# Optimization experiments

Hardware: AMD Instinct MI355X
Metric: run time of the kernel (lower is better)

The kernel has to match this reference:

```python
import jax, jax.numpy as jnp
import numpy as np

BIT = 8          # mantissa bits (incl. sign) for both weights and activations
BLK = 32         # block size along channel dim
QMAX = 2.0 ** (BIT - 1) - 1  # 127
EPS_BN = 1e-5


def bfp_quant(x, bit=BIT, blk=BLK):
    """BFPActivation: block-floating-point quantization of activations.
    Channels are grouped in blocks of `blk`; each block shares the exponent of
    its max-magnitude element, mantissas are rounded to `bit` bits (STE)."""
    N, C, H, W = x.shape
    xb = x.reshape(N, C // blk, blk, H, W)
    max_abs = jnp.max(jnp.abs(xb), axis=2, keepdims=True)
    e = jnp.floor(jnp.log2(jnp.maximum(max_abs, 1e-24)))  # shared exponent
    delta = jnp.exp2(e - (bit - 2))                        # quantization step
    q = jnp.clip(jnp.round(xb / delta), -(2.0 ** (bit - 1)), 2.0 ** (bit - 1) - 1) * delta
    q = q.reshape(N, C, H, W)
    return x + jax.lax.stop_gradient(q - x)  # straight-through


def w_quant(w, bit=BIT, blk=BLK):
    """DSConv2d weight quantization: per (out-channel, in-channel-block, kh, kw)
    float scale (KDS) with `bit`-bit integer mantissa (VQK)."""
    O, I, kh, kw = w.shape
    wb = w.reshape(O, I // blk, blk, kh, kw)
    alpha = jnp.maximum(jnp.max(jnp.abs(wb), axis=2, keepdims=True) / QMAX, 1e-24)
    q = (jnp.round(wb / alpha) * alpha).reshape(O, I, kh, kw)
    return w + jax.lax.stop_gradient(q - w)


def conv(x, w, stride=1, padding=0):
    return jax.lax.conv_general_dilated(
        x, w, (stride, stride), [(padding, padding)] * 2,
        dimension_numbers=("NCHW", "OIHW", "NCHW"))


def bn(x, g, b, m, v):
    # inference-mode BatchNorm2d with running stats
    inv = g / jnp.sqrt(v + EPS_BN)
    return x * inv[None, :, None, None] + (b - m * inv)[None, :, None, None]


def setup_inputs() -> dict:
    key = jax.random.key(0)
    ks = jax.random.split(key, 8)
    N, Cin, H, W_ = 64, 512, 28, 28
    width, Cout = 128, 512
    d = {}
    d["x"] = jax.random.normal(ks[0], (N, Cin, H, W_), jnp.float32)
    d["w1"] = jax.random.normal(ks[1], (width, Cin, 1, 1), jnp.float32) / np.sqrt(Cin)
    d["w2"] = jax.random.normal(ks[2], (width, width, 3, 3), jnp.float32) / np.sqrt(width * 9)
    d["w3"] = jax.random.normal(ks[3], (Cout, width, 1, 1), jnp.float32) / np.sqrt(width)
    for i, c in ((1, width), (2, width), (3, Cout)):
        kk = jax.random.split(jax.random.fold_in(key, i), 4)
        d[f"bn{i}_g"] = 1.0 + 0.1 * jax.random.normal(kk[0], (c,), jnp.float32)
        d[f"bn{i}_b"] = 0.1 * jax.random.normal(kk[1], (c,), jnp.float32)
        d[f"bn{i}_m"] = 0.1 * jax.random.normal(kk[2], (c,), jnp.float32)
        d[f"bn{i}_v"] = 0.5 + jax.random.uniform(kk[3], (c,), jnp.float32)
    return d


def reference(x, w1, w2, w3,
              bn1_g, bn1_b, bn1_m, bn1_v,
              bn2_g, bn2_b, bn2_m, bn2_v,
              bn3_g, bn3_b, bn3_m, bn3_v):
    identity = x
    out = conv(x, w_quant(w1))                       # 1x1, C 512->128
    out = bfp_quant(jax.nn.relu(bn(out, bn1_g, bn1_b, bn1_m, bn1_v)))
    out = conv(out, w_quant(w2), stride=1, padding=1)  # 3x3, C 128->128
    out = bfp_quant(jax.nn.relu(bn(out, bn2_g, bn2_b, bn2_m, bn2_v)))
    out = conv(out, w_quant(w3))                     # 1x1, C 128->512
    out = bn(out, bn3_g, bn3_b, bn3_m, bn3_v)
    out = out + identity
    # seq = Sequential(relu, activation2) in the source (final=False)
    out = bfp_quant(jax.nn.relu(out))
    return out
```

## Files before the change

### kernel.cpp

```cpp
#include <hip/hip_runtime.h>
#include <math.h>


#define HW 784
#define WW 28
#define PTOT 50176

typedef short s8v __attribute__((ext_vector_type(8)));
typedef float f4v __attribute__((ext_vector_type(4)));

__device__ __forceinline__ f4v mfma16(s8v a, s8v b, f4v c) {
  return __builtin_amdgcn_mfma_f32_16x16x32_bf16(a, b, c, 0, 0, 0);
}

__device__ __forceinline__ unsigned short f2bf(float f) {
  unsigned u = __float_as_uint(f);
  u += 0x7fffu + ((u >> 16) & 1u);
  return (unsigned short)(u >> 16);
}
__device__ __forceinline__ float bf2f(unsigned short h) {
  return __uint_as_float(((unsigned)h) << 16);
}

__global__ void wq1_kernel(const float* __restrict__ w, unsigned short* __restrict__ wd) {
  int task = blockIdx.x * blockDim.x + threadIdx.x;
  if (task >= 128 * 16) return;
  int cb = task & 15, o = task >> 4;
  const float* src = w + o * 512 + cb * 32;
  float vals[32], mx = 0.f;
#pragma unroll
  for (int j = 0; j < 32; ++j) { vals[j] = src[j]; mx = fmaxf(mx, fabsf(vals[j])); }
  float alpha = fmaxf(__fdiv_rn(mx, 127.0f), 1e-24f);
#pragma unroll
  for (int j = 0; j < 32; ++j) {
    unsigned short q = f2bf(__fmul_rn(rintf(__fdiv_rn(vals[j], alpha)), alpha));
    wd[o * 1024 + (cb * 32 + j) * 2] = q;
    wd[o * 1024 + (cb * 32 + j) * 2 + 1] = q;
  }
}

__global__ void wq2_kernel(const float* __restrict__ w, unsigned short* __restrict__ wd) {
  int task = blockIdx.x * blockDim.x + threadIdx.x;
  if (task >= 128 * 36) return;
  int o = task / 36, rem = task % 36;
  int khw = rem % 9, cb = rem / 9;
  float vals[32], mx = 0.f;
#pragma unroll
  for (int j = 0; j < 32; ++j) {
    vals[j] = w[(o * 128 + cb * 32 + j) * 9 + khw];
    mx = fmaxf(mx, fabsf(vals[j]));
  }
  float alpha = fmaxf(__fdiv_rn(mx, 127.0f), 1e-24f);
#pragma unroll
  for (int j = 0; j < 32; ++j)
    wd[o * 1152 + khw * 128 + cb * 32 + j] =
        f2bf(__fmul_rn(rintf(__fdiv_rn(vals[j], alpha)), alpha));
}

__global__ void wq3_kernel(const float* __restrict__ w, unsigned short* __restrict__ wd) {
  int task = blockIdx.x * blockDim.x + threadIdx.x;
  if (task >= 512 * 4) return;
  int cb = task & 3, o = task >> 2;
  const float* src = w + o * 128 + cb * 32;
  float vals[32], mx = 0.f;
#pragma unroll
  for (int j = 0; j < 32; ++j) { vals[j] = src[j]; mx = fmaxf(mx, fabsf(vals[j])); }
  float alpha = fmaxf(__fdiv_rn(mx, 127.0f), 1e-24f);
#pragma unroll
  for (int j = 0; j < 32; ++j)
    wd[o * 128 + cb * 32 + j] = f2bf(__fmul_rn(rintf(__fdiv_rn(vals[j], alpha)), alpha));
}

__global__ __launch_bounds__(256) void conv1_fused(
    const float* __restrict__ x, const unsigned short* __restrict__ Wq,
    const float* __restrict__ gg, const float* __restrict__ bb,
    const float* __restrict__ mm, const float* __restrict__ vv,
    unsigned short* __restrict__ out16) {
  __shared__ unsigned short As[64][72];

  const int t = threadIdx.x;
  const int w = t >> 6, l = t & 63;
  const int col = l & 15, row4 = l >> 4;
  const int P0 = blockIdx.x * 64;
  const int OG = w * 32;
  const int k0 = row4 * 8;

  const int p = P0 + l;
  const int n = p / HW;
  const int hw = p - n * HW;
  const float* xbase = x + (size_t)n * 512 * HW + hw;

  f4v acc[4][2];
#pragma unroll
  for (int pg = 0; pg < 4; ++pg)
#pragma unroll
    for (int og = 0; og < 2; ++og) acc[pg][og] = (f4v){0.f, 0.f, 0.f, 0.f};

  float xr[8];
#pragma unroll
  for (int j = 0; j < 8; ++j) xr[j] = xbase[(w * 8 + j) * HW];

  for (int s = 0; s < 16; ++s) {
    if (s) __syncthreads();
    s8v sv0, sv1;
#pragma unroll
    for (int j = 0; j < 4; ++j) {
      unsigned short hi = f2bf(xr[j]);
      float lo = __fsub_rn(xr[j], bf2f(hi));
      sv0[2 * j] = (short)hi;
      sv0[2 * j + 1] = (short)f2bf(lo);
    }
#pragma unroll
    for (int j = 0; j < 4; ++j) {
      unsigned short hi = f2bf(xr[4 + j]);
      float lo = __fsub_rn(xr[4 + j], bf2f(hi));
      sv1[2 * j] = (short)hi;
      sv1[2 * j + 1] = (short)f2bf(lo);
    }
    *(s8v*)&As[l][w * 16] = sv0;
    *(s8v*)&As[l][w * 16 + 8] = sv1;
    __syncthreads();
    if (s < 15) {
#pragma unroll
      for (int j = 0; j < 8; ++j) xr[j] = xbase[((s + 1) * 32 + w * 8 + j) * HW];
    }
#pragma unroll
    for (int kk = 0; kk < 2; ++kk) {
      s8v b0 = *(const s8v*)(Wq + (size_t)(OG + col) * 1024 + s * 64 + kk * 32 + k0);
      s8v b1 = *(const s8v*)(Wq + (size_t)(OG + 16 + col) * 1024 + s * 64 + kk * 32 + k0);
#pragma unroll
      for (int pg = 0; pg < 4; ++pg) {
        s8v af = *(const s8v*)&As[pg * 16 + col][kk * 32 + k0];
        acc[pg][0] = mfma16(af, b0, acc[pg][0]);
        acc[pg][1] = mfma16(af, b1, acc[pg][1]);
      }
    }
  }

  float inv_[2], ct_[2];
#pragma unroll
  for (int og = 0; og < 2; ++og) {
    int o = OG + og * 16 + col;
    float iv = __fdiv_rn(gg[o], sqrtf(__fadd_rn(vv[o], 1e-5f)));
    inv_[og] = iv;
    ct_[og] = __fsub_rn(bb[o], __fmul_rn(mm[o], iv));
  }
#pragma unroll
  for (int pg = 0; pg < 4; ++pg) {
#pragma unroll
    for (int r = 0; r < 4; ++r) {
      const int px = P0 + pg * 16 + row4 * 4 + r;
      float v0 = __fadd_rn(__fmul_rn(acc[pg][0][r], inv_[0]), ct_[0]);
      float v1 = __fadd_rn(__fmul_rn(acc[pg][1][r], inv_[1]), ct_[1]);
      v0 = fmaxf(v0, 0.f);
      v1 = fmaxf(v1, 0.f);
      float mx = fmaxf(v0, v1);
#pragma unroll
      for (int sfl = 1; sfl < 16; sfl <<= 1) mx = fmaxf(mx, __shfl_xor(mx, sfl));
      mx = fmaxf(mx, 1e-24f);
      int e = (int)(__float_as_uint(mx) >> 23) - 127;
      float dlt = __uint_as_float((unsigned)(e - 6 + 127) << 23);
      float idlt = __uint_as_float((unsigned)(6 - e + 127) << 23);
      float q0 = fminf(fmaxf(rintf(__fmul_rn(v0, idlt)), -128.f), 127.f);
      float q1 = fminf(fmaxf(rintf(__fmul_rn(v1, idlt)), -128.f), 127.f);
      out16[(size_t)px * 128 + OG + col] = f2bf(__fmul_rn(q0, dlt));
      out16[(size_t)px * 128 + OG + 16 + col] = f2bf(__fmul_rn(q1, dlt));
    }
  }
}

__global__ __launch_bounds__(256) void conv2_im2col(
    const unsigned short* __restrict__ A, const unsigned short* __restrict__ Wq,
    const float* __restrict__ gg, const float* __restrict__ bb,
    const float* __restrict__ mm, const float* __restrict__ vv,
    unsigned short* __restrict__ out16, const unsigned short* __restrict__ zp) {
  const int t = threadIdx.x;
  const int w = t >> 6, l = t & 63;
  const int col = l & 15, row4 = l >> 4;
  const int P0 = blockIdx.x * 64;
  const int OG = w * 32;
  const int k0 = row4 * 8;

  const unsigned short* bbase[2];
#pragma unroll
  for (int og = 0; og < 2; ++og)
    bbase[og] = Wq + (size_t)(OG + og * 16 + col) * 1152 + k0;

  f4v acc[4][2];
#pragma unroll
  for (int pg = 0; pg < 4; ++pg)
#pragma unroll
    for (int og = 0; og < 2; ++og) acc[pg][og] = (f4v){0.f, 0.f, 0.f, 0.f};

  int hh[4], wl[4], nb[4];
#pragma unroll
  for (int pg = 0; pg < 4; ++pg) {
    int p = P0 + pg * 16 + col;
    int n = p / HW, hw = p - n * HW;
    hh[pg] = hw / WW;
    wl[pg] = hw - hh[pg] * WW;
    nb[pg] = n * HW;
  }
#pragma unroll
  for (int ty = 0; ty < 3; ++ty)
#pragma unroll
    for (int tx = 0; tx < 3; ++tx) {
      const int tap = ty * 3 + tx;
      const unsigned short* ab[4];
#pragma unroll
      for (int pg = 0; pg < 4; ++pg) {
        int h2 = hh[pg] + ty - 1, w2 = wl[pg] + tx - 1;
        bool ok = ((unsigned)h2 < 28u) & ((unsigned)w2 < 28u);
        ab[pg] = ok ? (A + (size_t)(nb[pg] + h2 * WW + w2) * 128 + k0) : (zp + k0);
      }
#pragma unroll
      for (int cb = 0; cb < 4; ++cb) {
        s8v bf0 = *(const s8v*)(bbase[0] + tap * 128 + cb * 32);
        s8v bf1 = *(const s8v*)(bbase[1] + tap * 128 + cb * 32);
#pragma unroll
        for (int pg = 0; pg < 4; ++pg) {
          s8v af = *(const s8v*)(ab[pg] + cb * 32);
          acc[pg][0] = mfma16(af, bf0, acc[pg][0]);
          acc[pg][1] = mfma16(af, bf1, acc[pg][1]);
        }
      }
    }

  float inv_[2], ct_[2];
#pragma unroll
  for (int og = 0; og < 2; ++og) {
    int o = OG + og * 16 + col;
    float iv = __fdiv_rn(gg[o], sqrtf(__fadd_rn(vv[o], 1e-5f)));
    inv_[og] = iv;
    ct_[og] = __fsub_rn(bb[o], __fmul_rn(mm[o], iv));
  }
#pragma unroll
  for (int pg = 0; pg < 4; ++pg) {
#pragma unroll
    for (int r = 0; r < 4; ++r) {
      const int px = P0 + pg * 16 + row4 * 4 + r;
      float v0 = __fadd_rn(__fmul_rn(acc[pg][0][r], inv_[0]), ct_[0]);
      float v1 = __fadd_rn(__fmul_rn(acc[pg][1][r], inv_[1]), ct_[1]);
      v0 = fmaxf(v0, 0.f);
      v1 = fmaxf(v1, 0.f);
      float mx = fmaxf(v0, v1);
#pragma unroll
      for (int sfl = 1; sfl < 16; sfl <<= 1) mx = fmaxf(mx, __shfl_xor(mx, sfl));
      mx = fmaxf(mx, 1e-24f);
      int e = (int)(__float_as_uint(mx) >> 23) - 127;
      float dlt = __uint_as_float((unsigned)(e - 6 + 127) << 23);
      float idlt = __uint_as_float((unsigned)(6 - e + 127) << 23);
      float q0 = fminf(fmaxf(rintf(__fmul_rn(v0, idlt)), -128.f), 127.f);
      float q1 = fminf(fmaxf(rintf(__fmul_rn(v1, idlt)), -128.f), 127.f);
      out16[(size_t)px * 128 + OG + col] = f2bf(__fmul_rn(q0, dlt));
      out16[(size_t)px * 128 + OG + 16 + col] = f2bf(__fmul_rn(q1, dlt));
    }
  }
}

__global__ __launch_bounds__(256) void conv3_res(
    const unsigned short* __restrict__ A, const unsigned short* __restrict__ Wq,
    const float* __restrict__ gg, const float* __restrict__ bb,
    const float* __restrict__ mm, const float* __restrict__ vv,
    const float* __restrict__ resid, float* __restrict__ outf) {
  const int t = threadIdx.x;
  const int w = t >> 6, l = t & 63;
  const int col = l & 15, row4 = l >> 4;
  const int P0 = blockIdx.x * 64;
  const int OG = blockIdx.y * 128 + w * 32;
  const int k0 = row4 * 8;

  const unsigned short* ab[4];
#pragma unroll
  for (int pg = 0; pg < 4; ++pg)
    ab[pg] = A + (size_t)(P0 + pg * 16 + col) * 128 + k0;
  const unsigned short* b0p = Wq + (size_t)(OG + col) * 128 + k0;
  const unsigned short* b1p = Wq + (size_t)(OG + 16 + col) * 128 + k0;

  f4v acc[4][2];
#pragma unroll
  for (int pg = 0; pg < 4; ++pg)
#pragma unroll
    for (int og = 0; og < 2; ++og) acc[pg][og] = (f4v){0.f, 0.f, 0.f, 0.f};

#pragma unroll
  for (int kb = 0; kb < 4; ++kb) {
    s8v bf0 = *(const s8v*)(b0p + kb * 32);
    s8v bf1 = *(const s8v*)(b1p + kb * 32);
#pragma unroll
    for (int pg = 0; pg < 4; ++pg) {
      s8v af = *(const s8v*)(ab[pg] + kb * 32);
      acc[pg][0] = mfma16(af, bf0, acc[pg][0]);
      acc[pg][1] = mfma16(af, bf1, acc[pg][1]);
    }
  }

  float inv_[2], ct_[2];
#pragma unroll
  for (int og = 0; og < 2; ++og) {
    int o = OG + og * 16 + col;
    float iv = __fdiv_rn(gg[o], sqrtf(__fadd_rn(vv[o], 1e-5f)));
    inv_[og] = iv;
    ct_[og] = __fsub_rn(bb[o], __fmul_rn(mm[o], iv));
  }

#pragma unroll
  for (int pg = 0; pg < 4; ++pg) {
    const int px0 = P0 + pg * 16 + row4 * 4;
    const int n = px0 / HW;
    const int hw0 = px0 - n * HW;
    const size_t base0 = ((size_t)n * 512 + OG + col) * HW + hw0;
    const size_t base1 = ((size_t)n * 512 + OG + 16 + col) * HW + hw0;
    const float4 r0 = *(const float4*)(resid + base0);
    const float4 r1 = *(const float4*)(resid + base1);
    const float rr0[4] = {r0.x, r0.y, r0.z, r0.w};
    const float rr1[4] = {r1.x, r1.y, r1.z, r1.w};
    float s0[4], s1[4];
#pragma unroll
    for (int r = 0; r < 4; ++r) {
      float v0 = __fadd_rn(__fmul_rn(acc[pg][0][r], inv_[0]), ct_[0]);
      float v1 = __fadd_rn(__fmul_rn(acc[pg][1][r], inv_[1]), ct_[1]);
      v0 = __fadd_rn(v0, rr0[r]);
      v1 = __fadd_rn(v1, rr1[r]);
      v0 = fmaxf(v0, 0.f);
      v1 = fmaxf(v1, 0.f);
      float mx = fmaxf(v0, v1);
#pragma unroll
      for (int sfl = 1; sfl < 16; sfl <<= 1) mx = fmaxf(mx, __shfl_xor(mx, sfl));
      mx = fmaxf(mx, 1e-24f);
      int e = (int)(__float_as_uint(mx) >> 23) - 127;
      float dlt = __uint_as_float((unsigned)(e - 6 + 127) << 23);
      float idlt = __uint_as_float((unsigned)(6 - e + 127) << 23);
      float q0 = fminf(fmaxf(rintf(__fmul_rn(v0, idlt)), -128.f), 127.f);
      float q1 = fminf(fmaxf(rintf(__fmul_rn(v1, idlt)), -128.f), 127.f);
      s0[r] = __fmul_rn(q0, dlt);
      s1[r] = __fmul_rn(q1, dlt);
    }
    *(float4*)(outf + base0) = make_float4(s0[0], s0[1], s0[2], s0[3]);
    *(float4*)(outf + base1) = make_float4(s1[0], s1[1], s1[2], s1[3]);
  }
}

extern "C" void kernel_launch(void* const* d_in, const int* in_sizes, int n_in,
                              void* d_out, int out_size, void* d_ws, size_t ws_size,
                              hipStream_t stream) {
  (void)in_sizes; (void)n_in; (void)out_size; (void)ws_size;
  const float* x = (const float*)d_in[0];
  const float* w1 = (const float*)d_in[1];
  const float* w2 = (const float*)d_in[2];
  const float* w3 = (const float*)d_in[3];
  const float* bn1g = (const float*)d_in[4];
  const float* bn1b = (const float*)d_in[5];
  const float* bn1m = (const float*)d_in[6];
  const float* bn1v = (const float*)d_in[7];
  const float* bn2g = (const float*)d_in[8];
  const float* bn2b = (const float*)d_in[9];
  const float* bn2m = (const float*)d_in[10];
  const float* bn2v = (const float*)d_in[11];
  const float* bn3g = (const float*)d_in[12];
  const float* bn3b = (const float*)d_in[13];
  const float* bn3m = (const float*)d_in[14];
  const float* bn3v = (const float*)d_in[15];

  unsigned short* ws = (unsigned short*)d_ws;
  unsigned short* zp = ws;
  unsigned short* w1d = ws + 256;
  unsigned short* w2q = w1d + 128 * 1024;
  unsigned short* w3q = w2q + 128 * 1152;
  unsigned short* a1 = w3q + 512 * 128;
  unsigned short* a2 = a1 + (size_t)PTOT * 128;

  hipMemsetAsync(zp, 0, 512, stream);

  wq1_kernel<<<8, 256, 0, stream>>>(w1, w1d);
  wq2_kernel<<<18, 256, 0, stream>>>(w2, w2q);
  wq3_kernel<<<8, 256, 0, stream>>>(w3, w3q);

  conv1_fused<<<dim3(PTOT / 64, 1), 256, 0, stream>>>(
      x, w1d, bn1g, bn1b, bn1m, bn1v, a1);
  conv2_im2col<<<dim3(PTOT / 64, 1), 256, 0, stream>>>(
      a1, w2q, bn2g, bn2b, bn2m, bn2v, a2, zp);
  conv3_res<<<dim3(PTOT / 64, 4), 256, 0, stream>>>(
      a2, w3q, bn3g, bn3b, bn3m, bn3v, x, (float*)d_out);
}
```

Measured before the change: 396.1 us.

## Double-buffer conv1 LDS tile and software-pipeline conv2 im2col loads

conv1 now uses two LDS buffers that alternate per K-step, which removes the second barrier per iteration, and its occupancy hint rises to 3 blocks per SM. conv2's 36 tap/channel-block steps are flattened into a register double-buffered pipeline, so the next step's global loads are issued before the current step's MFMAs. Its block-to-pixel mapping is also permuted to change L2 locality. The cost is more registers, which under the min-blocks hint may cause spills.

```diff
diff --git a/kernel.cpp b/kernel.cpp
--- a/kernel.cpp
+++ b/kernel.cpp
@@ -71,12 +71,12 @@
     wd[o * 128 + cb * 32 + j] = f2bf(__fmul_rn(rintf(__fdiv_rn(vals[j], alpha)), alpha));
 }
 
-__global__ __launch_bounds__(256) void conv1_fused(
+__global__ __launch_bounds__(256, 3) void conv1_fused(
     const float* __restrict__ x, const unsigned short* __restrict__ Wq,
     const float* __restrict__ gg, const float* __restrict__ bb,
     const float* __restrict__ mm, const float* __restrict__ vv,
     unsigned short* __restrict__ out16) {
-  __shared__ unsigned short As[64][72];
+  __shared__ unsigned short As[2][64][72];
 
   const int t = threadIdx.x;
   const int w = t >> 6, l = t & 63;
@@ -100,8 +100,8 @@
 #pragma unroll
   for (int j = 0; j < 8; ++j) xr[j] = xbase[(w * 8 + j) * HW];
 
+#pragma unroll 2
   for (int s = 0; s < 16; ++s) {
-    if (s) __syncthreads();
     s8v sv0, sv1;
 #pragma unroll
     for (int j = 0; j < 4; ++j) {
@@ -117,8 +117,8 @@
       sv1[2 * j] = (short)hi;
       sv1[2 * j + 1] = (short)f2bf(lo);
     }
-    *(s8v*)&As[l][w * 16] = sv0;
-    *(s8v*)&As[l][w * 16 + 8] = sv1;
+    *(s8v*)&As[s & 1][l][w * 16] = sv0;
+    *(s8v*)&As[s & 1][l][w * 16 + 8] = sv1;
     __syncthreads();
     if (s < 15) {
 #pragma unroll
@@ -130,7 +130,7 @@
       s8v b1 = *(const s8v*)(Wq + (size_t)(OG + 16 + col) * 1024 + s * 64 + kk * 32 + k0);
 #pragma unroll
       for (int pg = 0; pg < 4; ++pg) {
-        s8v af = *(const s8v*)&As[pg * 16 + col][kk * 32 + k0];
+        s8v af = *(const s8v*)&As[s & 1][pg * 16 + col][kk * 32 + k0];
         acc[pg][0] = mfma16(af, b0, acc[pg][0]);
         acc[pg][1] = mfma16(af, b1, acc[pg][1]);
       }
@@ -169,7 +169,35 @@
   }
 }
 
-__global__ __launch_bounds__(256) void conv2_im2col(
+#define C2_SETTAP(ty_, tx_)                                                  \
+  {                                                                          \
+    _Pragma("unroll") for (int pg = 0; pg < 4; ++pg) {                       \
+      int h2 = hh[pg] + (ty_)-1, w2 = wl[pg] + (tx_)-1;                      \
+      bool ok = ((unsigned)h2 < 28u) & ((unsigned)w2 < 28u);                 \
+      ap[pg] = ok ? (A + (size_t)(nb[pg] + h2 * WW + w2) * 128 + k0)         \
+                  : (zp + k0);                                               \
+    }                                                                        \
+  }
+
+#define C2_LOAD(Ab, Bb0, Bb1, s_)                                            \
+  {                                                                          \
+    const int tap_ = (s_) >> 2, cb_ = (s_)&3;                                \
+    if (cb_ == 0) C2_SETTAP(tap_ / 3, tap_ % 3);                             \
+    Bb0 = *(const s8v*)(bb0 + tap_ * 128 + cb_ * 32);                        \
+    Bb1 = *(const s8v*)(bb1 + tap_ * 128 + cb_ * 32);                        \
+    _Pragma("unroll") for (int pg = 0; pg < 4; ++pg)                         \
+        Ab[pg] = *(const s8v*)(ap[pg] + cb_ * 32);                           \
+  }
+
+#define C2_MFMA(Ab, Bb0, Bb1)                                                \
+  {                                                                          \
+    _Pragma("unroll") for (int pg = 0; pg < 4; ++pg) {                       \
+      acc[pg][0] = mfma16(Ab[pg], Bb0, acc[pg][0]);                          \
+      acc[pg][1] = mfma16(Ab[pg], Bb1, acc[pg][1]);                          \
+    }                                                                        \
+  }
+
+__global__ __launch_bounds__(256, 3) void conv2_im2col(
     const unsigned short* __restrict__ A, const unsigned short* __restrict__ Wq,
     const float* __restrict__ gg, const float* __restrict__ bb,
     const float* __restrict__ mm, const float* __restrict__ vv,
@@ -177,14 +205,13 @@
   const int t = threadIdx.x;
   const int w = t >> 6, l = t & 63;
   const int col = l & 15, row4 = l >> 4;
-  const int P0 = blockIdx.x * 64;
+  const int bid = blockIdx.x;
+  const int P0 = ((bid & 7) * 98 + (bid >> 3)) * 64;
   const int OG = w * 32;
   const int k0 = row4 * 8;
 
-  const unsigned short* bbase[2];
-#pragma unroll
-  for (int og = 0; og < 2; ++og)
-    bbase[og] = Wq + (size_t)(OG + og * 16 + col) * 1152 + k0;
+  const unsigned short* bb0 = Wq + (size_t)(OG + col) * 1152 + k0;
+  const unsigned short* bb1 = Wq + (size_t)(OG + 16 + col) * 1152 + k0;
 
   f4v acc[4][2];
 #pragma unroll
@@ -201,30 +228,17 @@
     wl[pg] = hw - hh[pg] * WW;
     nb[pg] = n * HW;
   }
-#pragma unroll
-  for (int ty = 0; ty < 3; ++ty)
-#pragma unroll
-    for (int tx = 0; tx < 3; ++tx) {
-      const int tap = ty * 3 + tx;
-      const unsigned short* ab[4];
-#pragma unroll
-      for (int pg = 0; pg < 4; ++pg) {
-        int h2 = hh[pg] + ty - 1, w2 = wl[pg] + tx - 1;
-        bool ok = ((unsigned)h2 < 28u) & ((unsigned)w2 < 28u);
-        ab[pg] = ok ? (A + (size_t)(nb[pg] + h2 * WW + w2) * 128 + k0) : (zp + k0);
-      }
-#pragma unroll
-      for (int cb = 0; cb < 4; ++cb) {
-        s8v bf0 = *(const s8v*)(bbase[0] + tap * 128 + cb * 32);
-        s8v bf1 = *(const s8v*)(bbase[1] + tap * 128 + cb * 32);
-#pragma unroll
-        for (int pg = 0; pg < 4; ++pg) {
-          s8v af = *(const s8v*)(ab[pg] + cb * 32);
-          acc[pg][0] = mfma16(af, bf0, acc[pg][0]);
-          acc[pg][1] = mfma16(af, bf1, acc[pg][1]);
-        }
-      }
-    }
+
+  const unsigned short* ap[4];
+  s8v A0[4], A1[4], B00, B01, B10, B11;
+  C2_LOAD(A0, B00, B01, 0);
+#pragma unroll
+  for (int ss = 0; ss < 18; ++ss) {
+    C2_LOAD(A1, B10, B11, 2 * ss + 1);
+    C2_MFMA(A0, B00, B01);
+    if (ss < 17) C2_LOAD(A0, B00, B01, 2 * ss + 2);
+    C2_MFMA(A1, B10, B11);
+  }
 
   float inv_[2], ct_[2];
 #pragma unroll
```

Result: faster. 380.6 us (-3.9%).
